# Kernel optimization log

Hardware: AMD Instinct MI355X
Metric: run time of the kernel (lower is better)

Reference implementation:

```python
import jax, jax.numpy as jnp
import numpy as np

L = 3          # num_layers
H = 128        # hidden_dim
DIN = 256      # input_dim
DE = 64        # edge_dim
DOUT = 128     # output_dim
MSG_IN = 2 * H + DE + 3  # 323
N_GRAPHS = 64
BN_EPS = 1e-5


def _bn_eval(x, g, b):
    # eval-mode BatchNorm1d with running_mean=0, running_var=1
    return x * (g / jnp.sqrt(1.0 + BN_EPS)) + b


def setup_inputs() -> dict:
    key = jax.random.key(0)
    ks = jax.random.split(key, 32)
    N, E = 50000, 400000
    inp = {
        "x": jax.random.normal(ks[0], (N, DIN), jnp.float32),
        "edge_index": jax.random.randint(ks[1], (2, E), 0, N, jnp.int64),
        "edge_attr": jax.random.normal(ks[2], (E, DE), jnp.float32),
        "pos": jax.random.normal(ks[3], (N, 3), jnp.float32),
        "batch": jnp.sort(jax.random.randint(ks[4], (N,), 0, N_GRAPHS, jnp.int64)),
    }
    s = 0.02
    inp["Wi"] = jax.random.normal(ks[5], (DIN, H), jnp.float32) * s
    inp["bi"] = jnp.zeros((H,), jnp.float32)
    inp["node_W"] = jax.random.normal(ks[6], (L, H, H), jnp.float32) * s
    inp["node_b"] = jnp.zeros((L, H), jnp.float32)
    inp["msg_W1"] = jax.random.normal(ks[7], (L, MSG_IN, H), jnp.float32) * s
    inp["msg_b1"] = jnp.zeros((L, H), jnp.float32)
    inp["msg_g"] = jnp.ones((L, H), jnp.float32)
    inp["msg_be"] = jnp.zeros((L, H), jnp.float32)
    inp["msg_W2"] = jax.random.normal(ks[8], (L, H, H), jnp.float32) * s
    inp["msg_b2"] = jnp.zeros((L, H), jnp.float32)
    inp["out_W1"] = jax.random.normal(ks[9], (H, H), jnp.float32) * s
    inp["out_b1"] = jnp.zeros((H,), jnp.float32)
    inp["out_g"] = jnp.ones((H,), jnp.float32)
    inp["out_be"] = jnp.zeros((H,), jnp.float32)
    inp["out_W2"] = jax.random.normal(ks[10], (H, DOUT), jnp.float32) * s
    inp["out_b2"] = jnp.zeros((DOUT,), jnp.float32)
    return inp


def reference(x, edge_index, edge_attr, pos, batch,
              Wi, bi, node_W, node_b,
              msg_W1, msg_b1, msg_g, msg_be, msg_W2, msg_b2,
              out_W1, out_b1, out_g, out_be, out_W2, out_b2):
    N = x.shape[0]
    h = x @ Wi + bi                                   # [N, H]

    # add self loops once (same augmented graph every layer)
    loops = jnp.arange(N)
    src = jnp.concatenate([edge_index[0], loops])      # [E+N]
    dst = jnp.concatenate([edge_index[1], loops])      # [E+N]
    ea = jnp.concatenate(
        [edge_attr, jnp.zeros((N, edge_attr.shape[1]), edge_attr.dtype)], axis=0)

    rel_pos = pos[dst] - pos[src]                      # [E+N, 3] (zero on loops)

    for l in range(L):
        x_i = h[dst]                                   # target gather
        x_j = h[src]                                   # source gather
        m = jnp.concatenate([x_i, x_j, ea, rel_pos], axis=1)  # [E+N, 323]
        m = m @ msg_W1[l] + msg_b1[l]
        m = jax.nn.relu(_bn_eval(m, msg_g[l], msg_be[l]))
        m = m @ msg_W2[l] + msg_b2[l]
        aggr = jax.ops.segment_sum(m, dst, num_segments=N)    # scatter-add
        upd = jax.nn.relu(h @ node_W[l] + node_b[l] + aggr)   # update()
        h = h + upd                                    # residual in MPNN.forward

    # global mean pool over batch segments
    sums = jax.ops.segment_sum(h, batch, num_segments=N_GRAPHS)
    cnts = jax.ops.segment_sum(jnp.ones((N,), h.dtype), batch, num_segments=N_GRAPHS)
    pooled = sums / jnp.maximum(cnts, 1.0)[:, None]    # [G, H]

    o = pooled @ out_W1 + out_b1
    o = jax.nn.relu(_bn_eval(o, out_g, out_be))
    return o @ out_W2 + out_b2                         # [G, DOUT]
```

## Files before the change

### kernel.cpp

```cpp
#include <hip/hip_runtime.h>
#include <hip/hip_bf16.h>

#define NN     50000
#define NE     400000
#define NEA    450000
#define HD     128
#define DIN    256
#define DE     64
#define MSGIN  323
#define NG     64
#define NB     196

#define BN_RN 0.9999950000374997f

typedef __hip_bfloat16 bf16;

__device__ float ldv(const float* p, int i) { return p[i]; }
__device__ float ldv(const bf16* p, int i)  { return __bfloat162float(p[i]); }
__device__ void  stv(float* p, int i, float v) { p[i] = v; }
__device__ void  stv(bf16* p, int i, float v)  { p[i] = __float2bfloat16(v); }

__device__ int idx_is_i64(const int* p)
{
    return (p[1] | p[3] | p[5] | p[7]) == 0;
}

__device__ void atomic_add_f(float* addr, float val)
{
    unsigned int* p = (unsigned int*)addr;
    unsigned int old = *p;
    unsigned int assumed;
    do {
        assumed = old;
        float f = __uint_as_float(assumed) + val;
        old = atomicCAS(p, assumed, __float_as_uint(f));
    } while (old != assumed);
}

#define FMA4(A, sx, W) { (A).x += (sx)*(W).x; (A).y += (sx)*(W).y; \
                         (A).z += (sx)*(W).z; (A).w += (sx)*(W).w; }

__device__ void decode_edge(const int* ei, int i64, int i, int* ps, int* pd)
{
    int s, d;
    if (i < NE) {
        if (i64) { s = ei[2 * i]; d = ei[2 * (NE + i)]; }
        else     { s = ei[i];     d = ei[NE + i]; }
        if (s < 0 || s >= NN || d < 0 || d >= NN) { s = 0; d = -1; }
    } else {
        s = i - NE;
        d = s;
    }
    *ps = s; *pd = d;
}

__global__ void detect_kernel(const unsigned int* gones, int* flag)
{
    if (blockIdx.x == 0 && threadIdx.x == 0)
        flag[0] = (gones[0] == 0x3F800000u) ? 1 : 0;
}

__global__ void zero_kernel(float* p, int n)
{
    int i = blockIdx.x * blockDim.x + threadIdx.x;
    int stride = gridDim.x * blockDim.x;
    while (i < n) { p[i] = 0.0f; i += stride; }
}

__global__ void fill_f32_kernel(float* p, int n, float v)
{
    int i = blockIdx.x * blockDim.x + threadIdx.x;
    int stride = gridDim.x * blockDim.x;
    while (i < n) { p[i] = v; i += stride; }
}

__global__ void fill_out_kernel(bf16* out, int n, float v)
{
    int i = blockIdx.x * blockDim.x + threadIdx.x;
    if (i < n) out[i] = __float2bfloat16(v);
}

__global__ void deg_kernel(const int* ei, float* deg)
{
    int i = blockIdx.x * blockDim.x + threadIdx.x;
    int stride = gridDim.x * blockDim.x;
    int i64 = idx_is_i64(ei);
    while (i < NE) {
        int s, d;
        if (i64) { s = ei[2 * i]; d = ei[2 * (NE + i)]; }
        else     { s = ei[i];     d = ei[NE + i]; }
        if (s >= 0 && s < NN && d >= 0 && d < NN)
            unsafeAtomicAdd(&deg[d], 1.0f);
        i += stride;
    }
}

__global__ void hist_kernel(const int* ei, int* cnt)
{
    int i = blockIdx.x * blockDim.x + threadIdx.x;
    int stride = gridDim.x * blockDim.x;
    int i64 = idx_is_i64(ei);
    while (i < NEA) {
        int s, d;
        decode_edge(ei, i64, i, &s, &d);
        if (d >= 0) atomicAdd(&cnt[d], 1);
        i += stride;
    }
}

__global__ void scan1_kernel(const int* cnt, int* rowptr, int* bsum)
{
    __shared__ int sh[256];
    int t = threadIdx.x;
    int i = blockIdx.x * 256 + t;
    int v = (i < NN) ? cnt[i] : 0;
    sh[t] = v;
    __syncthreads();
    for (int off = 1; off < 256; off <<= 1) {
        int x = 0;
        if (t >= off) x = sh[t - off];
        __syncthreads();
        sh[t] += x;
        __syncthreads();
    }
    if (i < NN) rowptr[i] = sh[t] - v;
    if (t == 255) bsum[blockIdx.x] = sh[255];
}

__global__ void scan2_kernel(int* bsum, int nb)
{
    __shared__ int sh[256];
    int t = threadIdx.x;
    int v = (t < nb) ? bsum[t] : 0;
    sh[t] = v;
    __syncthreads();
    for (int off = 1; off < 256; off <<= 1) {
        int x = 0;
        if (t >= off) x = sh[t - off];
        __syncthreads();
        sh[t] += x;
        __syncthreads();
    }
    if (t == nb - 1) bsum[nb] = sh[t];
    if (t < nb) bsum[t] = sh[t] - v;
}

__global__ void scan3_kernel(int* rowptr, int* cursor, float* deg,
                             const int* cnt, const int* bsum)
{
    int i = blockIdx.x * 256 + threadIdx.x;
    if (i < NN) {
        int r = rowptr[i] + bsum[blockIdx.x];
        rowptr[i] = r;
        cursor[i] = r;
        deg[i] = (float)cnt[i];
        if (i == NN - 1) rowptr[NN] = r + cnt[i];
    }
}

__global__ void scatter_kernel(const int* ei, int* cursor, int2* sd, int* eid)
{
    int i = blockIdx.x * blockDim.x + threadIdx.x;
    int stride = gridDim.x * blockDim.x;
    int i64 = idx_is_i64(ei);
    while (i < NEA) {
        int s, d;
        decode_edge(ei, i64, i, &s, &d);
        if (d >= 0) {
            int pos = atomicAdd(&cursor[d], 1);
            int2 v; v.x = s; v.y = d;
            sd[pos] = v;
            eid[pos] = i;
        }
        i += stride;
    }
}

template <typename T, typename HT>
__global__ void gemm_in_kernel(const T* x, const T* Wi, const T* bi,
                               HT* h, const int* flag)
{
    if (flag[0] != (int)(sizeof(T) == 4)) return;

    __shared__ float xs[32 * 33];
    __shared__ float ws[32 * 128];

    int tid = threadIdx.x;
    int r0  = blockIdx.x * 32;
    int c0  = tid & 31;
    int r4  = (tid >> 5) * 4;

    float acc[4][4];
    int i, j, kk, k0, idx;
    for (j = 0; j < 4; ++j)
        for (i = 0; i < 4; ++i) acc[j][i] = 0.0f;

    for (k0 = 0; k0 < DIN; k0 += 32) {
        for (idx = tid; idx < 32 * 32; idx += 256) {
            int r = idx >> 5;
            int k = idx & 31;
            int row = r0 + r;
            float v = 0.0f;
            if (row < NN) v = ldv(x, row * DIN + k0 + k);
            xs[r * 33 + k] = v;
        }
        for (idx = tid; idx < 32 * 128; idx += 256) {
            int k = idx >> 7;
            int c = idx & 127;
            ws[k * 128 + c] = ldv(Wi, (k0 + k) * HD + c);
        }
        __syncthreads();
        for (kk = 0; kk < 32; ++kk) {
            float w0 = ws[kk * 128 + c0];
            float w1 = ws[kk * 128 + c0 + 32];
            float w2 = ws[kk * 128 + c0 + 64];
            float w3 = ws[kk * 128 + c0 + 96];
            for (j = 0; j < 4; ++j) {
                float xv = xs[(r4 + j) * 33 + kk];
                acc[j][0] += xv * w0;
                acc[j][1] += xv * w1;
                acc[j][2] += xv * w2;
                acc[j][3] += xv * w3;
            }
        }
        __syncthreads();
    }
    for (j = 0; j < 4; ++j) {
        int row = r0 + r4 + j;
        if (row < NN) {
            for (i = 0; i < 4; ++i) {
                int c = c0 + 32 * i;
                stv(h, row * HD + c, acc[j][i] + ldv(bi, c));
            }
        }
    }
}

template <typename T>
__global__ void pq_kernel(const float* h, const T* W1, float* PQ,
                          const int* flag)
{
    if (flag[0] != (int)(sizeof(T) == 4)) return;

    __shared__ float xs[32 * 33];
    __shared__ float ws[32 * 256];

    int tid = threadIdx.x;
    int r0  = blockIdx.x * 32;
    int c0  = tid & 31;
    int r4  = (tid >> 5) * 4;
    int i, j, kk, k0, idx;

    float acc[4][8];
    for (j = 0; j < 4; ++j)
        for (i = 0; i < 8; ++i) acc[j][i] = 0.0f;

    for (k0 = 0; k0 < HD; k0 += 32) {
        for (idx = tid; idx < 32 * 32; idx += 256) {
            int r = idx >> 5;
            int k = idx & 31;
            int row = r0 + r;
            float v = 0.0f;
            if (row < NN) v = h[row * HD + k0 + k];
            xs[r * 33 + k] = v;
        }
        for (idx = tid; idx < 32 * 256; idx += 256) {
            int k = idx >> 8;
            int c = idx & 255;
            int wrow = (c < 128) ? (k0 + k) : (128 + k0 + k);
            ws[k * 256 + c] = ldv(W1, wrow * HD + (c & 127));
        }
        __syncthreads();
        for (kk = 0; kk < 32; ++kk) {
            float xv0 = xs[(r4 + 0) * 33 + kk];
            float xv1 = xs[(r4 + 1) * 33 + kk];
            float xv2 = xs[(r4 + 2) * 33 + kk];
            float xv3 = xs[(r4 + 3) * 33 + kk];
            for (i = 0; i < 8; ++i) {
                float w = ws[kk * 256 + c0 + 32 * i];
                acc[0][i] += xv0 * w;
                acc[1][i] += xv1 * w;
                acc[2][i] += xv2 * w;
                acc[3][i] += xv3 * w;
            }
        }
        __syncthreads();
    }
    for (j = 0; j < 4; ++j) {
        int row = r0 + r4 + j;
        if (row < NN) {
            for (i = 0; i < 8; ++i)
                PQ[row * 256 + c0 + 32 * i] = acc[j][i];
        }
    }
}

template <typename T>
__global__ void edge_csr_kernel(const float* PQ, const int2* sd,
                                const int* eid, const int* rowptr,
                                const T* eattr, const T* pos,
                                const T* W1, const T* b1,
                                const T* g1, const T* be1,
                                float* S, const int* flag)
{
    if (flag[0] != (int)(sizeof(T) == 4)) return;

    __shared__ float ea_s[67 * 68];
    __shared__ float w_s[67 * 128];
    __shared__ int   src_s[64];
    __shared__ int   dst_s[64];
    __shared__ int   eid_s[64];
    __shared__ int   ve_s;

    int tid = threadIdx.x;
    int p0  = blockIdx.x * 64;
    int j, kk, idx;

    if (tid == 0) ve_s = rowptr[NN];
    __syncthreads();
    int VE = ve_s;
    if (p0 >= VE) return;

    if (tid < 64) {
        int p = p0 + tid;
        int s = 0, d = -1, e = 0;
        if (p < VE) {
            int2 v = sd[p];
            s = v.x; d = v.y;
            e = eid[p];
        }
        src_s[tid] = s;
        dst_s[tid] = d;
        eid_s[tid] = e;
    }
    __syncthreads();

    for (idx = tid; idx < 64 * 64; idx += 256) {
        int k = idx & 63;
        int r = idx >> 6;
        int e = eid_s[r];
        float v = 0.0f;
        if (dst_s[r] >= 0 && e < NE) v = ldv(eattr, e * DE + k);
        ea_s[k * 68 + r] = v;
    }
    if (tid < 64) {
        int e = eid_s[tid];
        int s = src_s[tid];
        int d = dst_s[tid];
        for (j = 0; j < 3; ++j) {
            float v = 0.0f;
            if (d >= 0 && e < NE)
                v = ldv(pos, d * 3 + j) - ldv(pos, s * 3 + j);
            ea_s[(64 + j) * 68 + tid] = v;
        }
    }
    for (idx = tid; idx < 67 * 128; idx += 256) {
        int k = idx >> 7;
        int c = idx & 127;
        int wrow = (k < 64) ? (256 + k) : (320 + (k - 64));
        w_s[idx] = ldv(W1, wrow * HD + c);
    }
    __syncthreads();

    int c0 = tid & 31;
    int g  = tid >> 5;
    int r8 = g * 8;
    int g2 = g * 2;

    float4 a0 = {0,0,0,0}, a1 = {0,0,0,0}, a2 = {0,0,0,0}, a3 = {0,0,0,0};
    float4 a4 = {0,0,0,0}, a5 = {0,0,0,0}, a6 = {0,0,0,0}, a7 = {0,0,0,0};

    {
        const float4* ea4 = (const float4*)ea_s;
        const float4* w4  = (const float4*)w_s;
        for (kk = 0; kk < 67; ++kk) {
            float4 wv = w4[kk * 32 + c0];
            float4 xa = ea4[kk * 17 + g2];
            float4 xb = ea4[kk * 17 + g2 + 1];
            FMA4(a0, xa.x, wv); FMA4(a1, xa.y, wv);
            FMA4(a2, xa.z, wv); FMA4(a3, xa.w, wv);
            FMA4(a4, xb.x, wv); FMA4(a5, xb.y, wv);
            FMA4(a6, xb.z, wv); FMA4(a7, xb.w, wv);
        }
    }
    __syncthreads();

    {
        float4* t4 = (float4*)w_s;
        t4[(r8 + 0) * 32 + c0] = a0;
        t4[(r8 + 1) * 32 + c0] = a1;
        t4[(r8 + 2) * 32 + c0] = a2;
        t4[(r8 + 3) * 32 + c0] = a3;
        t4[(r8 + 4) * 32 + c0] = a4;
        t4[(r8 + 5) * 32 + c0] = a5;
        t4[(r8 + 6) * 32 + c0] = a6;
        t4[(r8 + 7) * 32 + c0] = a7;
    }
    __syncthreads();

    {
        int c    = tid & 127;
        int rbeg = (tid >> 7) * 32;
        float b1c = ldv(b1, c);
        float gc  = ldv(g1, c) * BN_RN;
        float bec = ldv(be1, c);

        float run = 0.0f;
        int   dprev = -1;
        float pd = 0.0f;
        for (int r = rbeg; r < rbeg + 32; ++r) {
            int d = dst_s[r];
            if (d < 0) break;
            if (d != dprev) {
                if (dprev >= 0 && run != 0.0f)
                    unsafeAtomicAdd(&S[(size_t)dprev * HD + c], run);
                run = 0.0f;
                dprev = d;
                pd = PQ[(size_t)d * 256 + c];
            }
            int s = src_s[r];
            float pre = w_s[r * 128 + c] + pd
                      + PQ[(size_t)s * 256 + 128 + c] + b1c;
            float t = pre * gc + bec;
            if (t > 0.0f) run += t;
        }
        if (dprev >= 0 && run != 0.0f)
            unsafeAtomicAdd(&S[(size_t)dprev * HD + c], run);
    }
}

template <typename T>
__global__ void edge_kernel(const float* PQ, const int* ei,
                            const T* eattr, const T* pos,
                            const T* W1, const T* b1,
                            const T* g1, const T* be1,
                            float* S, const int* flag)
{
    if (flag[0] != (int)(sizeof(T) == 4)) return;

    __shared__ float ea_s[67 * 68];
    __shared__ float w_s[67 * 128];
    __shared__ int   src_s[64];
    __shared__ int   dst_s[64];

    int tid = threadIdx.x;
    int e0  = blockIdx.x * 64;
    int c0  = tid & 31;
    int g   = tid >> 5;
    int r8  = g * 8;
    int i, j, kk, idx;

    if (tid < 64) {
        int e = e0 + tid;
        int s = 0;
        int d = -1;
        if (e < NEA) {
            int i64 = idx_is_i64(ei);
            decode_edge(ei, i64, e, &s, &d);
        }
        src_s[tid] = s;
        dst_s[tid] = d;
    }
    __syncthreads();

    float4 a0 = {0,0,0,0}, a1 = {0,0,0,0}, a2 = {0,0,0,0}, a3 = {0,0,0,0};
    float4 a4 = {0,0,0,0}, a5 = {0,0,0,0}, a6 = {0,0,0,0}, a7 = {0,0,0,0};

    if (e0 < NE) {
        for (idx = tid; idx < 64 * 64; idx += 256) {
            int k = idx & 63;
            int r = idx >> 6;
            int e = e0 + r;
            float v = 0.0f;
            if (e < NE && dst_s[r] >= 0) v = ldv(eattr, e * DE + k);
            ea_s[k * 68 + r] = v;
        }
        if (tid < 64) {
            int e = e0 + tid;
            int s = src_s[tid];
            int d = dst_s[tid];
            for (j = 0; j < 3; ++j) {
                float v = 0.0f;
                if (e < NE && d >= 0)
                    v = ldv(pos, d * 3 + j) - ldv(pos, s * 3 + j);
                ea_s[(64 + j) * 68 + tid] = v;
            }
        }
        for (idx = tid; idx < 67 * 128; idx += 256) {
            int k = idx >> 7;
            int c = idx & 127;
            int wrow = (k < 64) ? (256 + k) : (320 + (k - 64));
            w_s[idx] = ldv(W1, wrow * HD + c);
        }
        __syncthreads();

        const float4* ea4 = (const float4*)ea_s;
        const float4* w4  = (const float4*)w_s;
        int g2 = g * 2;
        for (kk = 0; kk < 67; ++kk) {
            float4 wv = w4[kk * 32 + c0];
            float4 xa = ea4[kk * 17 + g2];
            float4 xb = ea4[kk * 17 + g2 + 1];
            FMA4(a0, xa.x, wv); FMA4(a1, xa.y, wv);
            FMA4(a2, xa.z, wv); FMA4(a3, xa.w, wv);
            FMA4(a4, xb.x, wv); FMA4(a5, xb.y, wv);
            FMA4(a6, xb.z, wv); FMA4(a7, xb.w, wv);
        }
    }
    __syncthreads();

    {
        float4* t4 = (float4*)w_s;
        t4[(r8 + 0) * 32 + c0] = a0;
        t4[(r8 + 1) * 32 + c0] = a1;
        t4[(r8 + 2) * 32 + c0] = a2;
        t4[(r8 + 3) * 32 + c0] = a3;
        t4[(r8 + 4) * 32 + c0] = a4;
        t4[(r8 + 5) * 32 + c0] = a5;
        t4[(r8 + 6) * 32 + c0] = a6;
        t4[(r8 + 7) * 32 + c0] = a7;
    }
    __syncthreads();

    for (i = 0; i < 4; ++i) {
        int c = c0 + 32 * i;
        float b1c = ldv(b1, c);
        float gc  = ldv(g1, c) * BN_RN;
        float bec = ldv(be1, c);
        for (j = 0; j < 8; ++j) {
            int rr = r8 + j;
            int d = dst_s[rr];
            if (d < 0) continue;
            int s = src_s[rr];
            float pre = w_s[rr * 128 + c] + PQ[d * 256 + c]
                      + PQ[s * 256 + 128 + c] + b1c;
            float t = pre * gc + bec;
            if (t > 0.0f)
                unsafeAtomicAdd(&S[d * HD + c], t);
        }
    }
}

template <typename T>
__global__ void node2_kernel(float* h, const float* S, const float* deg,
                             const T* W, const T* b,
                             const T* W2, const T* b2, const int* flag)
{
    if (flag[0] != (int)(sizeof(T) == 4)) return;

    __shared__ float xs[32 * 33];
    __shared__ float ws[32 * 128];

    int tid = threadIdx.x;
    int r0  = blockIdx.x * 32;
    int c0  = tid & 31;
    int r4  = (tid >> 5) * 4;
    int i, j, kk, k0, idx;

    float acc[4][4];
    for (j = 0; j < 4; ++j)
        for (i = 0; i < 4; ++i) acc[j][i] = 0.0f;

    for (k0 = 0; k0 < 256; k0 += 32) {
        for (idx = tid; idx < 32 * 32; idx += 256) {
            int r = idx >> 5;
            int k = idx & 31;
            int row = r0 + r;
            int kg = k0 + k;
            float v = 0.0f;
            if (row < NN)
                v = (kg < 128) ? h[row * HD + kg] : S[row * HD + (kg - 128)];
            xs[r * 33 + k] = v;
        }
        for (idx = tid; idx < 32 * 128; idx += 256) {
            int k = idx >> 7;
            int c = idx & 127;
            int kg = k0 + k;
            float v;
            if (kg < 128) v = ldv(W, kg * HD + c);
            else          v = ldv(W2, (kg - 128) * HD + c);
            ws[k * 128 + c] = v;
        }
        __syncthreads();
        for (kk = 0; kk < 32; ++kk) {
            float w0 = ws[kk * 128 + c0];
            float w1 = ws[kk * 128 + c0 + 32];
            float w2 = ws[kk * 128 + c0 + 64];
            float w3 = ws[kk * 128 + c0 + 96];
            for (j = 0; j < 4; ++j) {
                float xv = xs[(r4 + j) * 33 + kk];
                acc[j][0] += xv * w0;
                acc[j][1] += xv * w1;
                acc[j][2] += xv * w2;
                acc[j][3] += xv * w3;
            }
        }
        __syncthreads();
    }
    for (j = 0; j < 4; ++j) {
        int row = r0 + r4 + j;
        if (row < NN) {
            float dg = deg[row];
            for (i = 0; i < 4; ++i) {
                int c = c0 + 32 * i;
                float u = acc[j][i] + ldv(b, c) + dg * ldv(b2, c);
                if (u < 0.0f) u = 0.0f;
                h[row * HD + c] += u;
            }
        }
    }
}

template <typename T, typename HT>
__global__ void msg_kernel(const HT* h, const int* ei,
                           const T* eattr, const T* pos,
                           const T* W1, const T* b1,
                           const T* g1, const T* be1,
                           const T* W2, const T* b2,
                           float* aggr, const int* flag)
{
    if (flag[0] != (int)(sizeof(T) == 4)) return;

    __shared__ float in_s[32 * 325];
    __shared__ float w_s[32 * 128];
    __shared__ int   src_s[32];
    __shared__ int   dst_s[32];

    int tid = threadIdx.x;
    int e0  = blockIdx.x * 32;
    int c0  = tid & 31;
    int r4  = (tid >> 5) * 4;
    int i, j, kk, k0, idx;

    if (tid < 32) {
        int e = e0 + tid;
        int s = 0;
        int d = -1;
        if (e < NEA) {
            int i64 = idx_is_i64(ei);
            decode_edge(ei, i64, e, &s, &d);
        }
        src_s[tid] = s;
        dst_s[tid] = d;
    }
    __syncthreads();

    for (idx = tid; idx < 32 * 324; idx += 256) {
        int r = idx / 324;
        int k = idx - r * 324;
        int s = src_s[r];
        int d = dst_s[r];
        float v = 0.0f;
        if (d >= 0 && k < MSGIN) {
            if (k < 128) {
                v = ldv(h, d * HD + k);
            } else if (k < 256) {
                v = ldv(h, s * HD + (k - 128));
            } else if (k < 320) {
                int e = e0 + r;
                if (e < NE) v = ldv(eattr, e * DE + (k - 256));
            } else {
                int e = e0 + r;
                if (e < NE) v = ldv(pos, d * 3 + (k - 320)) - ldv(pos, s * 3 + (k - 320));
            }
        }
        in_s[r * 325 + k] = v;
    }

    float acc[4][4];
    for (j = 0; j < 4; ++j)
        for (i = 0; i < 4; ++i) acc[j][i] = ldv(b1, c0 + 32 * i);

    for (k0 = 0; k0 < MSGIN; k0 += 32) {
        int kc = MSGIN - k0;
        if (kc > 32) kc = 32;
        for (idx = tid; idx < 32 * 128; idx += 256) {
            int k = idx >> 7;
            int c = idx & 127;
            float v = 0.0f;
            if (k0 + k < MSGIN) v = ldv(W1, (k0 + k) * HD + c);
            w_s[k * 128 + c] = v;
        }
        __syncthreads();
        for (kk = 0; kk < kc; ++kk) {
            float w0 = w_s[kk * 128 + c0];
            float w1 = w_s[kk * 128 + c0 + 32];
            float w2 = w_s[kk * 128 + c0 + 64];
            float w3 = w_s[kk * 128 + c0 + 96];
            for (j = 0; j < 4; ++j) {
                float xv = in_s[(r4 + j) * 325 + k0 + kk];
                acc[j][0] += xv * w0;
                acc[j][1] += xv * w1;
                acc[j][2] += xv * w2;
                acc[j][3] += xv * w3;
            }
        }
        __syncthreads();
    }

    for (j = 0; j < 4; ++j) {
        for (i = 0; i < 4; ++i) {
            int c = c0 + 32 * i;
            float t = acc[j][i] * (ldv(g1, c) * BN_RN) + ldv(be1, c);
            if (t < 0.0f) t = 0.0f;
            in_s[(r4 + j) * 128 + c] = t;
        }
    }
    __syncthreads();

    float acc2[4][4];
    for (j = 0; j < 4; ++j)
        for (i = 0; i < 4; ++i) acc2[j][i] = ldv(b2, c0 + 32 * i);

    for (k0 = 0; k0 < HD; k0 += 32) {
        for (idx = tid; idx < 32 * 128; idx += 256) {
            int k = idx >> 7;
            int c = idx & 127;
            w_s[k * 128 + c] = ldv(W2, (k0 + k) * HD + c);
        }
        __syncthreads();
        for (kk = 0; kk < 32; ++kk) {
            float w0 = w_s[kk * 128 + c0];
            float w1 = w_s[kk * 128 + c0 + 32];
            float w2 = w_s[kk * 128 + c0 + 64];
            float w3 = w_s[kk * 128 + c0 + 96];
            for (j = 0; j < 4; ++j) {
                float xv = in_s[(r4 + j) * 128 + k0 + kk];
                acc2[j][0] += xv * w0;
                acc2[j][1] += xv * w1;
                acc2[j][2] += xv * w2;
                acc2[j][3] += xv * w3;
            }
        }
        __syncthreads();
    }

    for (j = 0; j < 4; ++j) {
        int d = dst_s[r4 + j];
        if (d >= 0) {
            for (i = 0; i < 4; ++i) {
                atomic_add_f(&aggr[d * HD + c0 + 32 * i], acc2[j][i]);
            }
        }
    }
}

template <typename T, typename HT>
__global__ void node_kernel(HT* h, const float* aggr,
                            const T* W, const T* b, const int* flag)
{
    if (flag[0] != (int)(sizeof(T) == 4)) return;

    __shared__ float xs[32 * 33];
    __shared__ float ws[32 * 128];

    int tid = threadIdx.x;
    int r0  = blockIdx.x * 32;
    int c0  = tid & 31;
    int r4  = (tid >> 5) * 4;
    int i, j, kk, k0, idx;

    float acc[4][4];
    for (j = 0; j < 4; ++j)
        for (i = 0; i < 4; ++i) acc[j][i] = 0.0f;

    for (k0 = 0; k0 < HD; k0 += 32) {
        for (idx = tid; idx < 32 * 32; idx += 256) {
            int r = idx >> 5;
            int k = idx & 31;
            int row = r0 + r;
            float v = 0.0f;
            if (row < NN) v = ldv(h, row * HD + k0 + k);
            xs[r * 33 + k] = v;
        }
        for (idx = tid; idx < 32 * 128; idx += 256) {
            int k = idx >> 7;
            int c = idx & 127;
            ws[k * 128 + c] = ldv(W, (k0 + k) * HD + c);
        }
        __syncthreads();
        for (kk = 0; kk < 32; ++kk) {
            float w0 = ws[kk * 128 + c0];
            float w1 = ws[kk * 128 + c0 + 32];
            float w2 = ws[kk * 128 + c0 + 64];
            float w3 = ws[kk * 128 + c0 + 96];
            for (j = 0; j < 4; ++j) {
                float xv = xs[(r4 + j) * 33 + kk];
                acc[j][0] += xv * w0;
                acc[j][1] += xv * w1;
                acc[j][2] += xv * w2;
                acc[j][3] += xv * w3;
            }
        }
        __syncthreads();
    }
    for (j = 0; j < 4; ++j) {
        int row = r0 + r4 + j;
        if (row < NN) {
            for (i = 0; i < 4; ++i) {
                int c = c0 + 32 * i;
                float u = acc[j][i] + ldv(b, c) + aggr[row * HD + c];
                if (u < 0.0f) u = 0.0f;
                stv(h, row * HD + c, ldv(h, row * HD + c) + u);
            }
        }
    }
}

template <typename T>
__global__ void pool_final2(const float* h, const int* batch,
                            const int* ei,
                            const T* W1, const T* b1,
                            const T* g1, const T* be1,
                            const T* W2, const T* b2,
                            T* out, const int* flag)
{
    if (flag[0] != (int)(sizeof(T) == 4)) return;

    __shared__ float s1[256];
    __shared__ float sm[128];
    __shared__ float sa[128];
    __shared__ int   range[2];

    int gidx = blockIdx.x;
    int tid  = threadIdx.x;
    int c    = tid & 127;
    int half = tid >> 7;
    int k;

    if (tid < 2) {
        int i64 = idx_is_i64(ei);
        int target = gidx + tid;
        int lo = 0;
        int hi = NN;
        while (lo < hi) {
            int mid = (lo + hi) >> 1;
            int bv;
            if (i64) bv = batch[2 * mid]; else bv = batch[mid];
            if (bv < target) lo = mid + 1; else hi = mid;
        }
        range[tid] = lo;
    }
    __syncthreads();

    int lo = range[0];
    int hi = range[1];
    float sum = 0.0f;
    for (k = lo + half; k < hi; k += 2) sum += h[(size_t)k * HD + c];
    s1[half * 128 + c] = sum;
    __syncthreads();

    if (tid < 128) {
        float cn = (float)(hi - lo);
        if (cn < 1.0f) cn = 1.0f;
        sm[c] = (s1[c] + s1[128 + c]) / cn;
    }
    __syncthreads();

    float a = 0.0f;
    for (k = half * 64; k < half * 64 + 64; ++k)
        a += sm[k] * ldv(W1, k * HD + c);
    s1[half * 128 + c] = a;
    __syncthreads();

    if (tid < 128) {
        float v = s1[c] + s1[128 + c] + ldv(b1, c);
        v = v * (ldv(g1, c) * BN_RN) + ldv(be1, c);
        if (v < 0.0f) v = 0.0f;
        sa[c] = v;
    }
    __syncthreads();

    float o = 0.0f;
    for (k = half * 64; k < half * 64 + 64; ++k)
        o += sa[k] * ldv(W2, k * HD + c);
    s1[half * 128 + c] = o;
    __syncthreads();

    if (tid < 128)
        stv(out, gidx * HD + c, s1[c] + s1[128 + c] + ldv(b2, c));
}

template <typename T, typename HT>
__global__ void pool_final_kernel(const HT* h, const int* batch,
                                  const int* ei,
                                  const T* W1, const T* b1,
                                  const T* g1, const T* be1,
                                  const T* W2, const T* b2,
                                  T* out, const int* flag)
{
    if (flag[0] != (int)(sizeof(T) == 4)) return;

    __shared__ float s1[128];
    __shared__ float s2[128];
    __shared__ int   range[2];

    int g = blockIdx.x;
    int c = threadIdx.x;
    int k;

    if (c < 2) {
        int i64 = idx_is_i64(ei);
        int target = g + c;
        int lo = 0;
        int hi = NN;
        while (lo < hi) {
            int mid = (lo + hi) >> 1;
            int bv;
            if (i64) bv = batch[2 * mid]; else bv = batch[mid];
            if (bv < target) lo = mid + 1; else hi = mid;
        }
        range[c] = lo;
    }
    __syncthreads();

    int lo = range[0];
    int hi = range[1];
    float sum = 0.0f;
    for (k = lo; k < hi; ++k) sum += ldv(h, k * HD + c);
    float cn = (float)(hi - lo);
    if (cn < 1.0f) cn = 1.0f;
    s1[c] = sum / cn;
    __syncthreads();

    float a = ldv(b1, c);
    for (k = 0; k < HD; ++k) a += s1[k] * ldv(W1, k * HD + c);
    a = a * (ldv(g1, c) * BN_RN) + ldv(be1, c);
    if (a < 0.0f) a = 0.0f;
    s2[c] = a;
    __syncthreads();

    float o = ldv(b2, c);
    for (k = 0; k < HD; ++k) o += s2[k] * ldv(W2, k * HD + c);
    stv(out, g * HD + c, o);
}

template <typename T>
static void run_pipeline_csr(void* const* d_in, float* h, float* S, float* PQ,
                             const float* deg, const int2* sd, const int* eid,
                             const int* rowptr, int* flag,
                             void* d_out, hipStream_t stream)
{
    const T*   x      = (const T*)d_in[0];
    const int* ei     = (const int*)d_in[1];
    const T*   eattr  = (const T*)d_in[2];
    const T*   pos    = (const T*)d_in[3];
    const int* batch  = (const int*)d_in[4];
    const T*   Wi     = (const T*)d_in[5];
    const T*   bi     = (const T*)d_in[6];
    const T*   node_W = (const T*)d_in[7];
    const T*   node_b = (const T*)d_in[8];
    const T*   msg_W1 = (const T*)d_in[9];
    const T*   msg_b1 = (const T*)d_in[10];
    const T*   msg_g  = (const T*)d_in[11];
    const T*   msg_be = (const T*)d_in[12];
    const T*   msg_W2 = (const T*)d_in[13];
    const T*   msg_b2 = (const T*)d_in[14];
    const T*   out_W1 = (const T*)d_in[15];
    const T*   out_b1 = (const T*)d_in[16];
    const T*   out_g  = (const T*)d_in[17];
    const T*   out_be = (const T*)d_in[18];
    const T*   out_W2 = (const T*)d_in[19];
    const T*   out_b2 = (const T*)d_in[20];

    int gemm_blocks = (NN + 31) / 32;
    int edge_blocks = (NEA + 63) / 64;
    int l;

    gemm_in_kernel<T, float><<<gemm_blocks, 256, 0, stream>>>(x, Wi, bi, h, flag);

    for (l = 0; l < 3; ++l) {
        zero_kernel<<<1024, 256, 0, stream>>>(S, NN * HD);
        pq_kernel<T><<<gemm_blocks, 256, 0, stream>>>(
            h, msg_W1 + (size_t)l * MSGIN * HD, PQ, flag);
        edge_csr_kernel<T><<<edge_blocks, 256, 0, stream>>>(
            PQ, sd, eid, rowptr, eattr, pos,
            msg_W1 + (size_t)l * MSGIN * HD, msg_b1 + (size_t)l * HD,
            msg_g + (size_t)l * HD, msg_be + (size_t)l * HD,
            S, flag);
        node2_kernel<T><<<gemm_blocks, 256, 0, stream>>>(
            h, S, deg,
            node_W + (size_t)l * HD * HD, node_b + (size_t)l * HD,
            msg_W2 + (size_t)l * HD * HD, msg_b2 + (size_t)l * HD, flag);
    }

    pool_final2<T><<<NG, 256, 0, stream>>>(
        h, batch, ei, out_W1, out_b1, out_g, out_be, out_W2, out_b2,
        (T*)d_out, flag);
}

template <typename T>
static void run_pipeline_new(void* const* d_in, float* h, float* S, float* PQ,
                             const float* deg, int* flag,
                             void* d_out, hipStream_t stream)
{
    const T*   x      = (const T*)d_in[0];
    const int* ei     = (const int*)d_in[1];
    const T*   eattr  = (const T*)d_in[2];
    const T*   pos    = (const T*)d_in[3];
    const int* batch  = (const int*)d_in[4];
    const T*   Wi     = (const T*)d_in[5];
    const T*   bi     = (const T*)d_in[6];
    const T*   node_W = (const T*)d_in[7];
    const T*   node_b = (const T*)d_in[8];
    const T*   msg_W1 = (const T*)d_in[9];
    const T*   msg_b1 = (const T*)d_in[10];
    const T*   msg_g  = (const T*)d_in[11];
    const T*   msg_be = (const T*)d_in[12];
    const T*   msg_W2 = (const T*)d_in[13];
    const T*   msg_b2 = (const T*)d_in[14];
    const T*   out_W1 = (const T*)d_in[15];
    const T*   out_b1 = (const T*)d_in[16];
    const T*   out_g  = (const T*)d_in[17];
    const T*   out_be = (const T*)d_in[18];
    const T*   out_W2 = (const T*)d_in[19];
    const T*   out_b2 = (const T*)d_in[20];

    int gemm_blocks = (NN + 31) / 32;
    int edge_blocks = (NEA + 63) / 64;
    int l;

    gemm_in_kernel<T, float><<<gemm_blocks, 256, 0, stream>>>(x, Wi, bi, h, flag);

    for (l = 0; l < 3; ++l) {
        zero_kernel<<<1024, 256, 0, stream>>>(S, NN * HD);
        pq_kernel<T><<<gemm_blocks, 256, 0, stream>>>(
            h, msg_W1 + (size_t)l * MSGIN * HD, PQ, flag);
        edge_kernel<T><<<edge_blocks, 256, 0, stream>>>(
            PQ, ei, eattr, pos,
            msg_W1 + (size_t)l * MSGIN * HD, msg_b1 + (size_t)l * HD,
            msg_g + (size_t)l * HD, msg_be + (size_t)l * HD,
            S, flag);
        node2_kernel<T><<<gemm_blocks, 256, 0, stream>>>(
            h, S, deg,
            node_W + (size_t)l * HD * HD, node_b + (size_t)l * HD,
            msg_W2 + (size_t)l * HD * HD, msg_b2 + (size_t)l * HD, flag);
    }

    pool_final2<T><<<NG, 256, 0, stream>>>(
        h, batch, ei, out_W1, out_b1, out_g, out_be, out_W2, out_b2,
        (T*)d_out, flag);
}

template <typename T, typename HT>
static void run_pipeline(void* const* d_in, HT* h, float* aggr, int* flag,
                         void* d_out, hipStream_t stream)
{
    const T*   x      = (const T*)d_in[0];
    const int* ei     = (const int*)d_in[1];
    const T*   eattr  = (const T*)d_in[2];
    const T*   pos    = (const T*)d_in[3];
    const int* batch  = (const int*)d_in[4];
    const T*   Wi     = (const T*)d_in[5];
    const T*   bi     = (const T*)d_in[6];
    const T*   node_W = (const T*)d_in[7];
    const T*   node_b = (const T*)d_in[8];
    const T*   msg_W1 = (const T*)d_in[9];
    const T*   msg_b1 = (const T*)d_in[10];
    const T*   msg_g  = (const T*)d_in[11];
    const T*   msg_be = (const T*)d_in[12];
    const T*   msg_W2 = (const T*)d_in[13];
    const T*   msg_b2 = (const T*)d_in[14];
    const T*   out_W1 = (const T*)d_in[15];
    const T*   out_b1 = (const T*)d_in[16];
    const T*   out_g  = (const T*)d_in[17];
    const T*   out_be = (const T*)d_in[18];
    const T*   out_W2 = (const T*)d_in[19];
    const T*   out_b2 = (const T*)d_in[20];

    int gemm_blocks = (NN + 31) / 32;
    int msg_blocks  = (NEA + 31) / 32;
    int l;

    gemm_in_kernel<T, HT><<<gemm_blocks, 256, 0, stream>>>(x, Wi, bi, h, flag);

    for (l = 0; l < 3; ++l) {
        zero_kernel<<<1024, 256, 0, stream>>>(aggr, NN * HD);
        msg_kernel<T, HT><<<msg_blocks, 256, 0, stream>>>(
            h, ei, eattr, pos,
            msg_W1 + (size_t)l * MSGIN * HD, msg_b1 + (size_t)l * HD,
            msg_g + (size_t)l * HD, msg_be + (size_t)l * HD,
            msg_W2 + (size_t)l * HD * HD, msg_b2 + (size_t)l * HD,
            aggr, flag);
        node_kernel<T, HT><<<gemm_blocks, 256, 0, stream>>>(
            h, aggr, node_W + (size_t)l * HD * HD, node_b + (size_t)l * HD, flag);
    }

    pool_final_kernel<T, HT><<<NG, 128, 0, stream>>>(
        h, batch, ei, out_W1, out_b1, out_g, out_be, out_W2, out_b2,
        (T*)d_out, flag);
}

extern "C" void kernel_launch(void* const* d_in, const int* in_sizes, int n_in,
                              void* d_out, int out_size, void* d_ws, size_t ws_size,
                              hipStream_t stream)
{
    const size_t AL = 256;
#define ALN(x) ((((size_t)(x)) + AL - 1) / AL * AL)

    const size_t hf32  = (size_t)NN * HD * 4;
    const size_t hb16  = (size_t)NN * HD * 2;
    const size_t sf32  = (size_t)NN * HD * 4;
    const size_t pqf32 = (size_t)NN * 256 * 4;
    const size_t degf  = (size_t)NN * 4;

    const size_t o_h    = 0;
    const size_t o_S    = o_h   + ALN(hf32);
    const size_t o_PQ   = o_S   + ALN(sf32);
    const size_t o_deg  = o_PQ  + ALN(pqf32);
    const size_t o_cnt  = o_deg + ALN(degf);
    const size_t o_row  = o_cnt + ALN((size_t)NN * 4);
    const size_t o_cur  = o_row + ALN((size_t)(NN + 1) * 4);
    const size_t o_bs   = o_cur + ALN((size_t)NN * 4);
    const size_t o_sd   = o_bs  + ALN((size_t)(NB + 1) * 4);
    const size_t o_eid  = o_sd  + ALN((size_t)NEA * 8);
    const size_t o_flg  = o_eid + ALN((size_t)NEA * 4);
    const size_t need_csr = o_flg + 64;

    const size_t need_new = hf32 + sf32 + pqf32 + degf + 64;
    const size_t need_f32 = hf32 + sf32 + 64;
    const size_t need_b16 = hb16 + sf32 + 64;

    int want_f32 = 1, want_b16 = 1;
    if (in_sizes && n_in > 11) {
        if (in_sizes[11] == 3 * HD * 4)      want_b16 = 0;
        else if (in_sizes[11] == 3 * HD * 2) want_f32 = 0;
    }

    char* base = (char*)d_ws;

    if (ws_size >= need_csr) {
        float* h      = (float*)(base + o_h);
        float* S      = (float*)(base + o_S);
        float* PQ     = (float*)(base + o_PQ);
        float* deg    = (float*)(base + o_deg);
        int*   cnt    = (int*)(base + o_cnt);
        int*   rowptr = (int*)(base + o_row);
        int*   cursor = (int*)(base + o_cur);
        int*   bsum   = (int*)(base + o_bs);
        int2*  sd     = (int2*)(base + o_sd);
        int*   eid    = (int*)(base + o_eid);
        int*   flag   = (int*)(base + o_flg);
        const int* ei = (const int*)d_in[1];

        detect_kernel<<<1, 1, 0, stream>>>((const unsigned int*)d_in[11], flag);

        zero_kernel<<<256, 256, 0, stream>>>((float*)cnt, NN);
        hist_kernel<<<1024, 256, 0, stream>>>(ei, cnt);
        scan1_kernel<<<NB, 256, 0, stream>>>(cnt, rowptr, bsum);
        scan2_kernel<<<1, 256, 0, stream>>>(bsum, NB);
        scan3_kernel<<<NB, 256, 0, stream>>>(rowptr, cursor, deg, cnt, bsum);
        scatter_kernel<<<1024, 256, 0, stream>>>(ei, cursor, sd, eid);

        if (want_f32)
            run_pipeline_csr<float>(d_in, h, S, PQ, deg, sd, eid, rowptr,
                                    flag, d_out, stream);
        if (want_b16)
            run_pipeline_csr<bf16>(d_in, h, S, PQ, deg, sd, eid, rowptr,
                                   flag, d_out, stream);
    } else if (ws_size >= need_new) {
        float* h    = (float*)d_ws;
        float* S    = (float*)((char*)d_ws + hf32);
        float* PQ   = (float*)((char*)d_ws + hf32 + sf32);
        float* deg  = (float*)((char*)d_ws + hf32 + sf32 + pqf32);
        int*   flag = (int*)((char*)d_ws + hf32 + sf32 + pqf32 + degf);

        detect_kernel<<<1, 1, 0, stream>>>((const unsigned int*)d_in[11], flag);
        fill_f32_kernel<<<256, 256, 0, stream>>>(deg, NN, 1.0f);
        deg_kernel<<<1024, 256, 0, stream>>>((const int*)d_in[1], deg);

        if (want_f32)
            run_pipeline_new<float>(d_in, h, S, PQ, deg, flag, d_out, stream);
        if (want_b16)
            run_pipeline_new<bf16>(d_in, h, S, PQ, deg, flag, d_out, stream);
    } else if (ws_size >= need_f32) {
        float* h    = (float*)d_ws;
        float* aggr = (float*)((char*)d_ws + hf32);
        int*   flag = (int*)((char*)d_ws + hf32 + sf32);

        detect_kernel<<<1, 1, 0, stream>>>((const unsigned int*)d_in[11], flag);
        if (want_f32)
            run_pipeline<float, float>(d_in, h, aggr, flag, d_out, stream);
        if (want_b16)
            run_pipeline<bf16,  float>(d_in, h, aggr, flag, d_out, stream);
    } else if (ws_size >= need_b16) {
        bf16*  h    = (bf16*)d_ws;
        float* aggr = (float*)((char*)d_ws + hb16);
        int*   flag = (int*)((char*)d_ws + hb16 + sf32);

        detect_kernel<<<1, 1, 0, stream>>>((const unsigned int*)d_in[11], flag);
        if (want_f32)
            run_pipeline<float, bf16>(d_in, h, aggr, flag, d_out, stream);
        if (want_b16)
            run_pipeline<bf16,  bf16>(d_in, h, aggr, flag, d_out, stream);
    } else {
        fill_out_kernel<<<(out_size + 255) / 256, 256, 0, stream>>>(
            (bf16*)d_out, out_size, 3.0f);
    }
#undef ALN
}
```

Measured before the change: 1.863 ms.

## Fuse S zeroing into PQ kernel, chunk edge weights, vectorize CSR epilogue

The S accumulator is now zeroed inside pq_kernel, which removes the separate zero_kernel launch each layer. The edge CSR kernel loads the 67x128 edge weight slice in two chunks of 34 rows, shrinking shared memory to allow more resident blocks. Its epilogue now works straight from registers in float4 form, with a running per-destination reduction, instead of staging through shared memory. The non-CSR fallback (edge_kernel, run_pipeline_new) is removed, and that workspace path now routes to the old run_pipeline. Chunking the weights adds extra barriers and reloads the weights per chunk.

```diff
diff --git a/kernel.cpp b/kernel.cpp
--- a/kernel.cpp
+++ b/kernel.cpp
@@ -238,7 +238,7 @@
 
 template <typename T>
 __global__ void pq_kernel(const float* h, const T* W1, float* PQ,
-                          const int* flag)
+                          float* S, const int* flag)
 {
     if (flag[0] != (int)(sizeof(T) == 4)) return;
 
@@ -250,6 +250,17 @@
     int c0  = tid & 31;
     int r4  = (tid >> 5) * 4;
     int i, j, kk, k0, idx;
+
+    {
+        float4 z = {0.0f, 0.0f, 0.0f, 0.0f};
+        float4* S4 = (float4*)S;
+        for (idx = tid; idx < 32 * 32; idx += 256) {
+            int r = idx >> 5;
+            int c = idx & 31;
+            int row = r0 + r;
+            if (row < NN) S4[(size_t)row * 32 + c] = z;
+        }
+    }
 
     float acc[4][8];
     for (j = 0; j < 4; ++j)
@@ -306,7 +317,7 @@
     if (flag[0] != (int)(sizeof(T) == 4)) return;
 
     __shared__ float ea_s[67 * 68];
-    __shared__ float w_s[67 * 128];
+    __shared__ float w_s[34 * 128];
     __shared__ int   src_s[64];
     __shared__ int   dst_s[64];
     __shared__ int   eid_s[64];
@@ -314,7 +325,7 @@
 
     int tid = threadIdx.x;
     int p0  = blockIdx.x * 64;
-    int j, kk, idx;
+    int j, kk, kc, idx;
 
     if (tid == 0) ve_s = rowptr[NN];
     __syncthreads();
@@ -354,13 +365,6 @@
             ea_s[(64 + j) * 68 + tid] = v;
         }
     }
-    for (idx = tid; idx < 67 * 128; idx += 256) {
-        int k = idx >> 7;
-        int c = idx & 127;
-        int wrow = (k < 64) ? (256 + k) : (320 + (k - 64));
-        w_s[idx] = ldv(W1, wrow * HD + c);
-    }
-    __syncthreads();
 
     int c0 = tid & 31;
     int g  = tid >> 5;
@@ -370,175 +374,80 @@
     float4 a0 = {0,0,0,0}, a1 = {0,0,0,0}, a2 = {0,0,0,0}, a3 = {0,0,0,0};
     float4 a4 = {0,0,0,0}, a5 = {0,0,0,0}, a6 = {0,0,0,0}, a7 = {0,0,0,0};
 
-    {
-        const float4* ea4 = (const float4*)ea_s;
-        const float4* w4  = (const float4*)w_s;
-        for (kk = 0; kk < 67; ++kk) {
-            float4 wv = w4[kk * 32 + c0];
-            float4 xa = ea4[kk * 17 + g2];
-            float4 xb = ea4[kk * 17 + g2 + 1];
-            FMA4(a0, xa.x, wv); FMA4(a1, xa.y, wv);
-            FMA4(a2, xa.z, wv); FMA4(a3, xa.w, wv);
-            FMA4(a4, xb.x, wv); FMA4(a5, xb.y, wv);
-            FMA4(a6, xb.z, wv); FMA4(a7, xb.w, wv);
-        }
-    }
-    __syncthreads();
-
-    {
-        float4* t4 = (float4*)w_s;
-        t4[(r8 + 0) * 32 + c0] = a0;
-        t4[(r8 + 1) * 32 + c0] = a1;
-        t4[(r8 + 2) * 32 + c0] = a2;
-        t4[(r8 + 3) * 32 + c0] = a3;
-        t4[(r8 + 4) * 32 + c0] = a4;
-        t4[(r8 + 5) * 32 + c0] = a5;
-        t4[(r8 + 6) * 32 + c0] = a6;
-        t4[(r8 + 7) * 32 + c0] = a7;
-    }
-    __syncthreads();
-
-    {
-        int c    = tid & 127;
-        int rbeg = (tid >> 7) * 32;
-        float b1c = ldv(b1, c);
-        float gc  = ldv(g1, c) * BN_RN;
-        float bec = ldv(be1, c);
-
-        float run = 0.0f;
-        int   dprev = -1;
-        float pd = 0.0f;
-        for (int r = rbeg; r < rbeg + 32; ++r) {
-            int d = dst_s[r];
-            if (d < 0) break;
-            if (d != dprev) {
-                if (dprev >= 0 && run != 0.0f)
-                    unsafeAtomicAdd(&S[(size_t)dprev * HD + c], run);
-                run = 0.0f;
-                dprev = d;
-                pd = PQ[(size_t)d * 256 + c];
-            }
-            int s = src_s[r];
-            float pre = w_s[r * 128 + c] + pd
-                      + PQ[(size_t)s * 256 + 128 + c] + b1c;
-            float t = pre * gc + bec;
-            if (t > 0.0f) run += t;
-        }
-        if (dprev >= 0 && run != 0.0f)
-            unsafeAtomicAdd(&S[(size_t)dprev * HD + c], run);
-    }
-}
-
-template <typename T>
-__global__ void edge_kernel(const float* PQ, const int* ei,
-                            const T* eattr, const T* pos,
-                            const T* W1, const T* b1,
-                            const T* g1, const T* be1,
-                            float* S, const int* flag)
-{
-    if (flag[0] != (int)(sizeof(T) == 4)) return;
-
-    __shared__ float ea_s[67 * 68];
-    __shared__ float w_s[67 * 128];
-    __shared__ int   src_s[64];
-    __shared__ int   dst_s[64];
-
-    int tid = threadIdx.x;
-    int e0  = blockIdx.x * 64;
-    int c0  = tid & 31;
-    int g   = tid >> 5;
-    int r8  = g * 8;
-    int i, j, kk, idx;
-
-    if (tid < 64) {
-        int e = e0 + tid;
-        int s = 0;
-        int d = -1;
-        if (e < NEA) {
-            int i64 = idx_is_i64(ei);
-            decode_edge(ei, i64, e, &s, &d);
-        }
-        src_s[tid] = s;
-        dst_s[tid] = d;
-    }
-    __syncthreads();
-
-    float4 a0 = {0,0,0,0}, a1 = {0,0,0,0}, a2 = {0,0,0,0}, a3 = {0,0,0,0};
-    float4 a4 = {0,0,0,0}, a5 = {0,0,0,0}, a6 = {0,0,0,0}, a7 = {0,0,0,0};
-
-    if (e0 < NE) {
-        for (idx = tid; idx < 64 * 64; idx += 256) {
-            int k = idx & 63;
-            int r = idx >> 6;
-            int e = e0 + r;
-            float v = 0.0f;
-            if (e < NE && dst_s[r] >= 0) v = ldv(eattr, e * DE + k);
-            ea_s[k * 68 + r] = v;
-        }
-        if (tid < 64) {
-            int e = e0 + tid;
-            int s = src_s[tid];
-            int d = dst_s[tid];
-            for (j = 0; j < 3; ++j) {
-                float v = 0.0f;
-                if (e < NE && d >= 0)
-                    v = ldv(pos, d * 3 + j) - ldv(pos, s * 3 + j);
-                ea_s[(64 + j) * 68 + tid] = v;
-            }
-        }
-        for (idx = tid; idx < 67 * 128; idx += 256) {
+    for (kc = 0; kc < 67; kc += 34) {
+        int kcnt = 67 - kc;
+        if (kcnt > 34) kcnt = 34;
+        for (idx = tid; idx < kcnt * 128; idx += 256) {
             int k = idx >> 7;
             int c = idx & 127;
-            int wrow = (k < 64) ? (256 + k) : (320 + (k - 64));
+            int krow = kc + k;
+            int wrow = (krow < 64) ? (256 + krow) : (320 + (krow - 64));
             w_s[idx] = ldv(W1, wrow * HD + c);
         }
         __syncthreads();
-
-        const float4* ea4 = (const float4*)ea_s;
-        const float4* w4  = (const float4*)w_s;
-        int g2 = g * 2;
-        for (kk = 0; kk < 67; ++kk) {
-            float4 wv = w4[kk * 32 + c0];
-            float4 xa = ea4[kk * 17 + g2];
-            float4 xb = ea4[kk * 17 + g2 + 1];
-            FMA4(a0, xa.x, wv); FMA4(a1, xa.y, wv);
-            FMA4(a2, xa.z, wv); FMA4(a3, xa.w, wv);
-            FMA4(a4, xb.x, wv); FMA4(a5, xb.y, wv);
-            FMA4(a6, xb.z, wv); FMA4(a7, xb.w, wv);
-        }
-    }
-    __syncthreads();
-
-    {
-        float4* t4 = (float4*)w_s;
-        t4[(r8 + 0) * 32 + c0] = a0;
-        t4[(r8 + 1) * 32 + c0] = a1;
-        t4[(r8 + 2) * 32 + c0] = a2;
-        t4[(r8 + 3) * 32 + c0] = a3;
-        t4[(r8 + 4) * 32 + c0] = a4;
-        t4[(r8 + 5) * 32 + c0] = a5;
-        t4[(r8 + 6) * 32 + c0] = a6;
-        t4[(r8 + 7) * 32 + c0] = a7;
-    }
-    __syncthreads();
-
-    for (i = 0; i < 4; ++i) {
-        int c = c0 + 32 * i;
-        float b1c = ldv(b1, c);
-        float gc  = ldv(g1, c) * BN_RN;
-        float bec = ldv(be1, c);
-        for (j = 0; j < 8; ++j) {
-            int rr = r8 + j;
-            int d = dst_s[rr];
-            if (d < 0) continue;
-            int s = src_s[rr];
-            float pre = w_s[rr * 128 + c] + PQ[d * 256 + c]
-                      + PQ[s * 256 + 128 + c] + b1c;
-            float t = pre * gc + bec;
-            if (t > 0.0f)
-                unsafeAtomicAdd(&S[d * HD + c], t);
-        }
-    }
+        {
+            const float4* ea4 = (const float4*)ea_s;
+            const float4* w4  = (const float4*)w_s;
+            for (kk = 0; kk < kcnt; ++kk) {
+                float4 wv = w4[kk * 32 + c0];
+                float4 xa = ea4[(kc + kk) * 17 + g2];
+                float4 xb = ea4[(kc + kk) * 17 + g2 + 1];
+                FMA4(a0, xa.x, wv); FMA4(a1, xa.y, wv);
+                FMA4(a2, xa.z, wv); FMA4(a3, xa.w, wv);
+                FMA4(a4, xb.x, wv); FMA4(a5, xb.y, wv);
+                FMA4(a6, xb.z, wv); FMA4(a7, xb.w, wv);
+            }
+        }
+        __syncthreads();
+    }
+
+    float4 b1v, gv, bev;
+    b1v.x = ldv(b1, 4 * c0 + 0); b1v.y = ldv(b1, 4 * c0 + 1);
+    b1v.z = ldv(b1, 4 * c0 + 2); b1v.w = ldv(b1, 4 * c0 + 3);
+    gv.x = ldv(g1, 4 * c0 + 0) * BN_RN; gv.y = ldv(g1, 4 * c0 + 1) * BN_RN;
+    gv.z = ldv(g1, 4 * c0 + 2) * BN_RN; gv.w = ldv(g1, 4 * c0 + 3) * BN_RN;
+    bev.x = ldv(be1, 4 * c0 + 0); bev.y = ldv(be1, 4 * c0 + 1);
+    bev.z = ldv(be1, 4 * c0 + 2); bev.w = ldv(be1, 4 * c0 + 3);
+
+    const float4* pq4 = (const float4*)PQ;
+    float4 run = {0.0f, 0.0f, 0.0f, 0.0f};
+    float4 pp  = {0.0f, 0.0f, 0.0f, 0.0f};
+    int dprev = -1;
+
+#define EDGE_FLUSH() { \
+    float* sr = &S[(size_t)dprev * HD + 4 * c0]; \
+    if (run.x > 0.0f) unsafeAtomicAdd(sr + 0, run.x); \
+    if (run.y > 0.0f) unsafeAtomicAdd(sr + 1, run.y); \
+    if (run.z > 0.0f) unsafeAtomicAdd(sr + 2, run.z); \
+    if (run.w > 0.0f) unsafeAtomicAdd(sr + 3, run.w); }
+
+#define EDGE_EPI(J, A) { \
+    int rr = r8 + (J); \
+    int d = dst_s[rr]; \
+    if (d >= 0) { \
+        if (d != dprev) { \
+            if (dprev >= 0) EDGE_FLUSH(); \
+            run.x = 0.0f; run.y = 0.0f; run.z = 0.0f; run.w = 0.0f; \
+            dprev = d; \
+            pp = pq4[(size_t)d * 64 + c0]; \
+        } \
+        int s = src_s[rr]; \
+        float4 qq = pq4[(size_t)s * 64 + 32 + c0]; \
+        float t0 = ((A).x + pp.x + qq.x + b1v.x) * gv.x + bev.x; \
+        float t1 = ((A).y + pp.y + qq.y + b1v.y) * gv.y + bev.y; \
+        float t2 = ((A).z + pp.z + qq.z + b1v.z) * gv.z + bev.z; \
+        float t3 = ((A).w + pp.w + qq.w + b1v.w) * gv.w + bev.w; \
+        if (t0 > 0.0f) run.x += t0; \
+        if (t1 > 0.0f) run.y += t1; \
+        if (t2 > 0.0f) run.z += t2; \
+        if (t3 > 0.0f) run.w += t3; \
+    } }
+
+    EDGE_EPI(0, a0) EDGE_EPI(1, a1) EDGE_EPI(2, a2) EDGE_EPI(3, a3)
+    EDGE_EPI(4, a4) EDGE_EPI(5, a5) EDGE_EPI(6, a6) EDGE_EPI(7, a7)
+    if (dprev >= 0) EDGE_FLUSH();
+#undef EDGE_EPI
+#undef EDGE_FLUSH
 }
 
 template <typename T>
@@ -970,9 +879,8 @@
     gemm_in_kernel<T, float><<<gemm_blocks, 256, 0, stream>>>(x, Wi, bi, h, flag);
 
     for (l = 0; l < 3; ++l) {
-        zero_kernel<<<1024, 256, 0, stream>>>(S, NN * HD);
         pq_kernel<T><<<gemm_blocks, 256, 0, stream>>>(
-            h, msg_W1 + (size_t)l * MSGIN * HD, PQ, flag);
+            h, msg_W1 + (size_t)l * MSGIN * HD, PQ, S, flag);
         edge_csr_kernel<T><<<edge_blocks, 256, 0, stream>>>(
             PQ, sd, eid, rowptr, eattr, pos,
             msg_W1 + (size_t)l * MSGIN * HD, msg_b1 + (size_t)l * HD,
@@ -989,10 +897,9 @@
         (T*)d_out, flag);
 }
 
-template <typename T>
-static void run_pipeline_new(void* const* d_in, float* h, float* S, float* PQ,
-                             const float* deg, int* flag,
-                             void* d_out, hipStream_t stream)
+template <typename T, typename HT>
+static void run_pipeline(void* const* d_in, HT* h, float* aggr, int* flag,
+                         void* d_out, hipStream_t stream)
 {
     const T*   x      = (const T*)d_in[0];
     const int* ei     = (const int*)d_in[1];
@@ -1017,58 +924,6 @@
     const T*   out_b2 = (const T*)d_in[20];
 
     int gemm_blocks = (NN + 31) / 32;
-    int edge_blocks = (NEA + 63) / 64;
-    int l;
-
-    gemm_in_kernel<T, float><<<gemm_blocks, 256, 0, stream>>>(x, Wi, bi, h, flag);
-
-    for (l = 0; l < 3; ++l) {
-        zero_kernel<<<1024, 256, 0, stream>>>(S, NN * HD);
-        pq_kernel<T><<<gemm_blocks, 256, 0, stream>>>(
-            h, msg_W1 + (size_t)l * MSGIN * HD, PQ, flag);
-        edge_kernel<T><<<edge_blocks, 256, 0, stream>>>(
-            PQ, ei, eattr, pos,
-            msg_W1 + (size_t)l * MSGIN * HD, msg_b1 + (size_t)l * HD,
-            msg_g + (size_t)l * HD, msg_be + (size_t)l * HD,
-            S, flag);
-        node2_kernel<T><<<gemm_blocks, 256, 0, stream>>>(
-            h, S, deg,
-            node_W + (size_t)l * HD * HD, node_b + (size_t)l * HD,
-            msg_W2 + (size_t)l * HD * HD, msg_b2 + (size_t)l * HD, flag);
-    }
-
-    pool_final2<T><<<NG, 256, 0, stream>>>(
-        h, batch, ei, out_W1, out_b1, out_g, out_be, out_W2, out_b2,
-        (T*)d_out, flag);
-}
-
-template <typename T, typename HT>
-static void run_pipeline(void* const* d_in, HT* h, float* aggr, int* flag,
-                         void* d_out, hipStream_t stream)
-{
-    const T*   x      = (const T*)d_in[0];
-    const int* ei     = (const int*)d_in[1];
-    const T*   eattr  = (const T*)d_in[2];
-    const T*   pos    = (const T*)d_in[3];
-    const int* batch  = (const int*)d_in[4];
-    const T*   Wi     = (const T*)d_in[5];
-    const T*   bi     = (const T*)d_in[6];
-    const T*   node_W = (const T*)d_in[7];
-    const T*   node_b = (const T*)d_in[8];
-    const T*   msg_W1 = (const T*)d_in[9];
-    const T*   msg_b1 = (const T*)d_in[10];
-    const T*   msg_g  = (const T*)d_in[11];
-    const T*   msg_be = (const T*)d_in[12];
-    const T*   msg_W2 = (const T*)d_in[13];
-    const T*   msg_b2 = (const T*)d_in[14];
-    const T*   out_W1 = (const T*)d_in[15];
-    const T*   out_b1 = (const T*)d_in[16];
-    const T*   out_g  = (const T*)d_in[17];
-    const T*   out_be = (const T*)d_in[18];
-    const T*   out_W2 = (const T*)d_in[19];
-    const T*   out_b2 = (const T*)d_in[20];
-
-    int gemm_blocks = (NN + 31) / 32;
     int msg_blocks  = (NEA + 31) / 32;
     int l;
 
@@ -1169,10 +1024,14 @@
         fill_f32_kernel<<<256, 256, 0, stream>>>(deg, NN, 1.0f);
         deg_kernel<<<1024, 256, 0, stream>>>((const int*)d_in[1], deg);
 
-        if (want_f32)
-            run_pipeline_new<float>(d_in, h, S, PQ, deg, flag, d_out, stream);
-        if (want_b16)
-            run_pipeline_new<bf16>(d_in, h, S, PQ, deg, flag, d_out, stream);
+        int gemm_blocks = (NN + 31) / 32;
+        (void)gemm_blocks;
+        if (want_f32) {
+            run_pipeline<float, float>(d_in, h, S, flag, d_out, stream);
+        }
+        if (want_b16) {
+            run_pipeline<bf16, float>(d_in, h, S, flag, d_out, stream);
+        }
     } else if (ws_size >= need_f32) {
         float* h    = (float*)d_ws;
         float* aggr = (float*)((char*)d_ws + hf32);
```

Result: faster. 1.645 ms (-11.7%).
